# Kernel optimization log

Hardware: AMD Instinct MI355X
Metric: run time of the kernel (lower is better)

Reference implementation:

```python
import jax, jax.numpy as jnp
import numpy as np
import math

EMBED_DIM = 1024
NUM_HEADS = 16
HEAD_DIM = EMBED_DIM // NUM_HEADS
ROPE_BASE = 10000.0


def _rope_cache(seq_len, dim, dtype=jnp.float32):
    inv_freq = 1.0 / (ROPE_BASE ** (jnp.arange(0, dim, 2, dtype=jnp.float32) / dim))
    t = jnp.arange(seq_len, dtype=jnp.float32)
    freqs = t[:, None] * inv_freq[None, :]          # [S, D/2]
    emb = jnp.concatenate([freqs, freqs], axis=-1)  # [S, D]
    return jnp.cos(emb).astype(dtype), jnp.sin(emb).astype(dtype)


def _rotate_half(x):
    x1, x2 = jnp.split(x, 2, axis=-1)
    return jnp.concatenate([-x2, x1], axis=-1)


def setup_inputs() -> dict:
    key = jax.random.key(0)
    ks = jax.random.split(key, 12)
    B, S, E = 2, 2048, EMBED_DIM
    s = 1.0 / math.sqrt(E)
    inp = {
        "query": jax.random.normal(ks[0], (B, S, E), jnp.float32),
        "key": jax.random.normal(ks[1], (B, S, E), jnp.float32),
        "value": jax.random.normal(ks[2], (B, S, E), jnp.float32),
        "Wq": jax.random.normal(ks[3], (E, E), jnp.float32) * s,
        "bq": jnp.zeros((E,), jnp.float32),
        "Wk": jax.random.normal(ks[4], (E, E), jnp.float32) * s,
        "bk": jnp.zeros((E,), jnp.float32),
        "Wv": jax.random.normal(ks[5], (E, E), jnp.float32) * s,
        "bv": jnp.zeros((E,), jnp.float32),
        "Wo": jax.random.normal(ks[6], (E, E), jnp.float32) * s,
        "bo": jnp.zeros((E,), jnp.float32),
    }
    return inp


def reference(query, key, value, Wq, bq, Wk, bk, Wv, bv, Wo, bo):
    B, S, E = query.shape
    H, D = NUM_HEADS, HEAD_DIM

    def proj(x, W, b):  # torch Linear: x @ W.T + b -> [B,H,S,D]
        return (x @ W.T + b).reshape(B, -1, H, D).transpose(0, 2, 1, 3)

    q = proj(query, Wq, bq)
    k = proj(key, Wk, bk)
    v = proj(value, Wv, bv)

    cos, sin = _rope_cache(S, D, q.dtype)  # [S, D]
    cos = cos[None, None]                  # [1,1,S,D]
    sin = sin[None, None]
    q = q * cos + _rotate_half(q) * sin
    k = k * cos + _rotate_half(k) * sin

    scale = 1.0 / math.sqrt(D)
    scores = jnp.einsum("bhsd,bhtd->bhst", q, k) * scale  # [B,H,S,S]
    causal = jnp.triu(jnp.ones((S, S), bool), k=1)
    scores = jnp.where(causal[None, None], -jnp.inf, scores)
    attn = jax.nn.softmax(scores, axis=-1)
    out = jnp.einsum("bhst,bhtd->bhsd", attn, v)           # [B,H,S,D]
    out = out.transpose(0, 2, 1, 3).reshape(B, S, E)
    return out @ Wo.T + bo
```

## Files before the change

kernel.cpp:

```cpp
#include <hip/hip_runtime.h>
#include <math.h>

typedef unsigned short u16;
typedef __attribute__((ext_vector_type(4))) float f32x4;
typedef __attribute__((ext_vector_type(8))) short bf16x8;

#define SEQ   2048
#define EMB   1024
#define NH    16
#define HD    64
#define MROWS 4096

__device__ __forceinline__ u16 f2b(float f) {
    unsigned u = __float_as_uint(f);
    u += 0x7fff + ((u >> 16) & 1);
    return (u16)(u >> 16);
}
__device__ __forceinline__ unsigned pack_bf16x2(float a, float b) {
    unsigned ua = __float_as_uint(a) + 0x8000u;
    unsigned ub = __float_as_uint(b) + 0x8000u;
    return __builtin_amdgcn_perm(ub, ua, 0x07060302u);
}
__device__ __forceinline__ void gld16(const u16* g, const u16* l) {
    __builtin_amdgcn_global_load_lds((const __attribute__((address_space(1))) void*)g,
                                     (__attribute__((address_space(3))) void*)l, 16, 0, 0);
}

struct F2BArgs { const float* s[7]; u16* d[7]; };

__global__ void k_f2b(F2BArgs a) {
    int id = blockIdx.x;
    const float* src; u16* dst; int base;
    if (id < 6144) {
        int z = id >> 11;
        src = a.s[z]; dst = a.d[z];
        base = (id & 2047) << 8;
    } else {
        int r = id - 6144;
        int z = 3 + (r >> 9);
        src = a.s[z]; dst = a.d[z];
        base = (r & 511) << 8;
    }
    int i = base + threadIdx.x;
    const float4* s4 = (const float4*)src;
    float4 x = s4[i * 2], y = s4[i * 2 + 1];
    union { u16 u[8]; uint4 v; } o;
    o.u[0] = f2b(x.x); o.u[1] = f2b(x.y); o.u[2] = f2b(x.z); o.u[3] = f2b(x.w);
    o.u[4] = f2b(y.x); o.u[5] = f2b(y.y); o.u[6] = f2b(y.z); o.u[7] = f2b(y.w);
    ((uint4*)dst)[i] = o.v;
}

struct GemmArgs {
    const u16* A; const u16* Bw; const float* bias; u16* Cb;
};

__global__ __launch_bounds__(512, 2) void k_gemm_qkv(GemmArgs g0, GemmArgs g1, GemmArgs g2) {
    __shared__ u16 sbuf[3][24576];

    int id = blockIdx.x;
    int x = id / 48;
    int rem = id % 48;
    int z = rem >> 4;
    int y = rem & 15;
    GemmArgs g = (z == 0) ? g0 : (z == 1 ? g1 : g2);

    int tid = threadIdx.x;
    int wave = tid >> 6, lane = tid & 63, quad = lane >> 4, l16 = lane & 15;
    int wm = wave >> 1, wn = wave & 1;
    int m0 = y * 256, n0 = x * 128;
    const int K = EMB;

    auto stage = [&](int k0, u16* buf) {
#pragma unroll
        for (int pp = 0; pp < 6; pp++) {
            int slot = pp * 512 + tid;
            const u16* gsrc;
            if (pp < 4) {
                int row = slot >> 3, p = slot & 7;
                int c = p ^ (row & 7);
                gsrc = g.A + (size_t)(m0 + row) * K + k0 + c * 8;
            } else {
                int s2 = slot - 2048;
                int row = s2 >> 3, p = s2 & 7;
                int c = p ^ (row & 7);
                gsrc = g.Bw + (size_t)(n0 + row) * K + k0 + c * 8;
            }
            gld16(gsrc, buf + slot * 8);
        }
    };

    f32x4 acc[4][4];
#pragma unroll
    for (int i = 0; i < 4; i++)
#pragma unroll
        for (int j = 0; j < 4; j++) acc[i][j] = (f32x4){0.f, 0.f, 0.f, 0.f};

    int nt = K >> 6;
    stage(0, &sbuf[0][0]);
    stage(64, &sbuf[1][0]);
    for (int t = 0; t < nt; ++t) {
        if (t < nt - 1) asm volatile("s_waitcnt vmcnt(6)" ::: "memory");
        else            asm volatile("s_waitcnt vmcnt(0)" ::: "memory");
        asm volatile("s_barrier" ::: "memory");
        if (t + 2 < nt) stage((t + 2) << 6, &sbuf[0][0] + ((t + 2) % 3) * 24576);

        const u16* Ab = &sbuf[0][0] + (t % 3) * 24576;
        const u16* Bb = Ab + 16384;
#pragma unroll
        for (int kk = 0; kk < 2; kk++) {
            bf16x8 af[4], bfr[4];
#pragma unroll
            for (int i = 0; i < 4; i++) {
                int row = wm * 64 + i * 16 + l16;
                af[i] = *(const bf16x8*)&Ab[row * 64 + (((kk << 2) | quad) ^ (row & 7)) * 8];
            }
#pragma unroll
            for (int j = 0; j < 4; j++) {
                int row = wn * 64 + j * 16 + l16;
                bfr[j] = *(const bf16x8*)&Bb[row * 64 + (((kk << 2) | quad) ^ (row & 7)) * 8];
            }
#pragma unroll
            for (int i = 0; i < 4; i++)
#pragma unroll
                for (int j = 0; j < 4; j++)
                    acc[i][j] = __builtin_amdgcn_mfma_f32_16x16x32_bf16(af[i], bfr[j], acc[i][j], 0, 0, 0);
        }
    }

    if (z < 2) {
        float qscale = (z == 0) ? 0.18033688011112042f : 1.0f;
#pragma unroll
        for (int j = 0; j < 2; j++) {
            int col1 = n0 + wn * 64 + j * 16 + l16;
            int dd1 = col1 & 63;
            int h = col1 >> 6;
            float inv = __expf(-(float)dd1 * 0.28782313662425575f);
            float b1 = g.bias[col1], b2 = g.bias[col1 + 32];
#pragma unroll
            for (int i = 0; i < 4; i++)
#pragma unroll
                for (int r = 0; r < 4; r++) {
                    int row = m0 + wm * 64 + i * 16 + quad * 4 + r;
                    int b = row >> 11, s = row & (SEQ - 1);
                    float sn, cs;
                    __sincosf((float)s * inv, &sn, &cs);
                    float x1 = acc[i][j][r] + b1;
                    float x2 = acc[i][j + 2][r] + b2;
                    size_t base = ((size_t)(b * NH + h) * SEQ + s) << 6;
                    g.Cb[base + dd1]      = f2b((x1 * cs - x2 * sn) * qscale);
                    g.Cb[base + dd1 + 32] = f2b((x2 * cs + x1 * sn) * qscale);
                }
        }
    } else {
        __syncthreads();
        u16* tr = &sbuf[0][0] + wave * 4096;
        int h = (n0 >> 6) + wn;
        int b = m0 >> 11;
        int s0 = (m0 & (SEQ - 1)) + wm * 64;
#pragma unroll
        for (int j = 0; j < 4; j++) {
            float bv = g.bias[n0 + wn * 64 + j * 16 + l16];
#pragma unroll
            for (int i = 0; i < 4; i++) {
                uint2 pk;
                pk.x = pack_bf16x2(acc[i][j][0] + bv, acc[i][j][1] + bv);
                pk.y = pack_bf16x2(acc[i][j][2] + bv, acc[i][j][3] + bv);
                int row = j * 16 + l16;
                int c4 = i * 4 + quad;
                *(uint2*)&tr[row * 64 + ((c4 ^ (row & 14)) << 2)] = pk;
            }
        }
        u16* dst = g.Cb + (((size_t)(b * NH + h) * HD) * SEQ) + s0;
#pragma unroll
        for (int ps = 0; ps < 8; ps++) {
            int d = ps * 8 + (lane >> 3);
            int c4 = (lane & 7) * 2;
            uint4 v = *(const uint4*)&tr[d * 64 + ((c4 ^ (d & 14)) << 2)];
            *(uint4*)&dst[(size_t)d * SEQ + c4 * 4] = v;
        }
    }
}

__global__ __launch_bounds__(256) void k_gemm_o(const u16* __restrict__ A,
                                                const u16* __restrict__ Bw,
                                                const float* __restrict__ bias,
                                                float* __restrict__ C) {
    __shared__ u16 sb[2][6144];
    int tid = threadIdx.x;
    int w = tid >> 6, lane = tid & 63, quad = lane >> 4, l16 = lane & 15;
    int y = blockIdx.x & 63, x = blockIdx.x >> 6;
    int m0 = y * 64, n0 = x * 128;
    const int K = EMB;

    auto stage = [&](int k0, u16* buf) {
#pragma unroll
        for (int pp = 0; pp < 3; pp++) {
            int slot = pp * 256 + tid;
            if (slot < 256) {
                int row = slot >> 2, p = slot & 3;
                int c = p ^ (row & 3);
                gld16(A + (size_t)(m0 + row) * K + k0 + c * 8, buf + slot * 8);
            } else {
                int s2 = slot - 256;
                int row = s2 >> 2, p = s2 & 3;
                int c = p ^ (row & 3);
                gld16(Bw + (size_t)(n0 + row) * K + k0 + c * 8, buf + 2048 + s2 * 8);
            }
        }
    };

    f32x4 acc[4][2];
#pragma unroll
    for (int i = 0; i < 4; i++)
#pragma unroll
        for (int j = 0; j < 2; j++) acc[i][j] = (f32x4){0.f, 0.f, 0.f, 0.f};

    int nk = K >> 5;
    stage(0, sb[0]);
    for (int ks = 0; ks < nk; ks++) {
        __syncthreads();
        if (ks + 1 < nk) stage((ks + 1) << 5, sb[(ks + 1) & 1]);
        const u16* Ab = sb[ks & 1];
        const u16* Bb = Ab + 2048;
        bf16x8 af[4], bf[2];
#pragma unroll
        for (int i = 0; i < 4; i++) {
            int row = i * 16 + l16;
            af[i] = *(const bf16x8*)&Ab[row * 32 + (quad ^ (row & 3)) * 8];
        }
#pragma unroll
        for (int j = 0; j < 2; j++) {
            int row = w * 32 + j * 16 + l16;
            bf[j] = *(const bf16x8*)&Bb[row * 32 + (quad ^ (row & 3)) * 8];
        }
#pragma unroll
        for (int i = 0; i < 4; i++)
#pragma unroll
            for (int j = 0; j < 2; j++)
                acc[i][j] = __builtin_amdgcn_mfma_f32_16x16x32_bf16(af[i], bf[j], acc[i][j], 0, 0, 0);
    }

#pragma unroll
    for (int i = 0; i < 4; i++)
#pragma unroll
        for (int r = 0; r < 4; r++) {
            int row = m0 + i * 16 + quad * 4 + r;
#pragma unroll
            for (int j = 0; j < 2; j++) {
                int col = n0 + w * 32 + j * 16 + l16;
                C[(size_t)row * EMB + col] = acc[i][j][r] + bias[col];
            }
        }
}

__global__ __launch_bounds__(512, 2) void k_attn(const u16* __restrict__ Q,
                                                 const u16* __restrict__ K,
                                                 const u16* __restrict__ Vt,
                                                 u16* __restrict__ O) {
    __shared__ u16 kv[4][8192];
    __shared__ u16 Pl[8][1024];
    int tid = threadIdx.x;
    int w = tid >> 6, lane = tid & 63, quad = lane >> 4, l16 = lane & 15;
    int pair = w & 3, par = w >> 2;
    int bh = blockIdx.x & 31;
    int qt = 15 - (blockIdx.x >> 5);
    int q0w = qt * 128 + pair * 32;

    const u16* Qb = Q + (size_t)bh * SEQ * HD;
    const u16* Kb = K + (size_t)bh * SEQ * HD;
    const u16* Vb = Vt + (size_t)bh * HD * SEQ;
    u16* pl = Pl[w];

    auto stage = [&](int t0, u16* buf) {
#pragma unroll
        for (int pp = 0; pp < 2; pp++) {
            int slot = pp * 512 + tid;
            int r = (slot >> 3) & 63;
            int p = slot & 7;
            int c = p ^ (r & 7);
            const u16* gsrc = (pp < 1) ? Kb + (size_t)(t0 + r) * HD + c * 8
                                       : Vb + (size_t)r * SEQ + t0 + c * 8;
            gld16(gsrc, buf + slot * 8);
        }
    };

    bf16x8 bq[2][2];
#pragma unroll
    for (int g = 0; g < 2; g++) {
        size_t base = (size_t)(q0w + g * 16 + l16) * HD + quad * 8;
        bq[g][0] = *(const bf16x8*)&Qb[base];
        bq[g][1] = *(const bf16x8*)&Qb[base + 32];
    }

    f32x4 o2[2][4];
#pragma unroll
    for (int g = 0; g < 2; g++)
#pragma unroll
        for (int jd = 0; jd < 4; jd++) o2[g][jd] = (f32x4){0.f, 0.f, 0.f, 0.f};
    float l_p[2] = {0.f, 0.f};

    int nsup = qt + 1;
    stage(0, kv[0]);
    stage(64, kv[2]);
    for (int k = 0; k < nsup; ++k) {
        __syncthreads();
        if (k + 1 < nsup) {
            stage((k + 1) * 128,      kv[(k + 1) & 1]);
            stage((k + 1) * 128 + 64, kv[2 + ((k + 1) & 1)]);
        }
        int t0 = k * 128 + par * 64;
        if (t0 > q0w + 31) continue;

        const u16* Kl = kv[par * 2 + (k & 1)];
        const u16* Vl = Kl + 4096;

        bf16x8 kf[4][2], vf[4][2];
#pragma unroll
        for (int mt = 0; mt < 4; mt++) {
            int row = mt * 16 + l16;
            kf[mt][0] = *(const bf16x8*)&Kl[row * 64 + (quad ^ (row & 7)) * 8];
            kf[mt][1] = *(const bf16x8*)&Kl[row * 64 + ((quad + 4) ^ (row & 7)) * 8];
            vf[mt][0] = *(const bf16x8*)&Vl[row * 64 + (quad ^ (row & 7)) * 8];
            vf[mt][1] = *(const bf16x8*)&Vl[row * 64 + ((quad + 4) ^ (row & 7)) * 8];
        }

#pragma unroll
        for (int g = 0; g < 2; g++) {
            int qmin = q0w + g * 16;
            if (t0 > qmin + 15) continue;

            f32x4 sc[4];
#pragma unroll
            for (int mt = 0; mt < 4; mt++) {
                sc[mt] = (f32x4){0.f, 0.f, 0.f, 0.f};
                sc[mt] = __builtin_amdgcn_mfma_f32_16x16x32_bf16(kf[mt][0], bq[g][0], sc[mt], 0, 0, 0);
                sc[mt] = __builtin_amdgcn_mfma_f32_16x16x32_bf16(kf[mt][1], bq[g][1], sc[mt], 0, 0, 0);
            }

            if (t0 + 63 > qmin) {
                int q = qmin + l16;
#pragma unroll
                for (int mt = 0; mt < 4; mt++)
#pragma unroll
                    for (int r = 0; r < 4; r++) {
                        int t = t0 + mt * 16 + quad * 4 + r;
                        if (t > q) sc[mt][r] = -INFINITY;
                    }
            }

            float rs = 0.f;
#pragma unroll
            for (int mt = 0; mt < 4; mt++)
#pragma unroll
                for (int r = 0; r < 4; r++) {
                    float p = __builtin_amdgcn_exp2f(sc[mt][r] - 64.f);
                    sc[mt][r] = p;
                    rs += p;
                }
            l_p[g] += rs;

#pragma unroll
            for (int mt = 0; mt < 4; mt++) {
                uint2 pk;
                pk.x = pack_bf16x2(sc[mt][0], sc[mt][1]);
                pk.y = pack_bf16x2(sc[mt][2], sc[mt][3]);
                int chunk = 2 * mt + (quad >> 1);
                *(uint2*)&pl[l16 * 64 + (chunk ^ (l16 & 7)) * 8 + (quad & 1) * 4] = pk;
            }

            bf16x8 pb0 = *(const bf16x8*)&pl[l16 * 64 + (quad ^ (l16 & 7)) * 8];
            bf16x8 pb1 = *(const bf16x8*)&pl[l16 * 64 + ((quad + 4) ^ (l16 & 7)) * 8];

#pragma unroll
            for (int jd = 0; jd < 4; jd++) {
                o2[g][jd] = __builtin_amdgcn_mfma_f32_16x16x32_bf16(vf[jd][0], pb0, o2[g][jd], 0, 0, 0);
                o2[g][jd] = __builtin_amdgcn_mfma_f32_16x16x32_bf16(vf[jd][1], pb1, o2[g][jd], 0, 0, 0);
            }
        }
    }

    __syncthreads();
    float* mp = (float*)&kv[0][0] + pair * 2176;
    if (par) {
#pragma unroll
        for (int g = 0; g < 2; g++) {
#pragma unroll
            for (int jd = 0; jd < 4; jd++)
                *(f32x4*)&mp[(g * 4 + jd) * 256 + lane * 4] = o2[g][jd];
            mp[2048 + g * 64 + lane] = l_p[g];
        }
    }
    __syncthreads();
    if (par) return;
#pragma unroll
    for (int g = 0; g < 2; g++) {
#pragma unroll
        for (int jd = 0; jd < 4; jd++)
            o2[g][jd] += *(const f32x4*)&mp[(g * 4 + jd) * 256 + lane * 4];
        l_p[g] += mp[2048 + g * 64 + lane];
    }

    u16* ep = ((u16*)&kv[0][0]) + 18432 + pair * 1216;
    int b = bh >> 4, h = bh & (NH - 1);
#pragma unroll
    for (int g = 0; g < 2; g++) {
        float l = l_p[g];
        l += __shfl_xor(l, 16, 64);
        l += __shfl_xor(l, 32, 64);
        float inv = 1.f / l;
#pragma unroll
        for (int jd = 0; jd < 4; jd++) {
            uint2 pk;
            pk.x = pack_bf16x2(o2[g][jd][0] * inv, o2[g][jd][1] * inv);
            pk.y = pack_bf16x2(o2[g][jd][2] * inv, o2[g][jd][3] * inv);
            *(uint2*)&ep[l16 * 72 + jd * 16 + quad * 4] = pk;
        }
        int row = lane >> 2, dc = (lane & 3) * 16;
        uint4 d0 = *(const uint4*)&ep[row * 72 + dc];
        uint4 d1 = *(const uint4*)&ep[row * 72 + dc + 8];
        int q = q0w + g * 16 + row;
        size_t addr = (size_t)(b * SEQ + q) * EMB + h * HD + dc;
        *(uint4*)&O[addr] = d0;
        *(uint4*)&O[addr + 8] = d1;
    }
}

extern "C" void kernel_launch(void* const* d_in, const int* in_sizes, int n_in,
                              void* d_out, int out_size, void* d_ws, size_t ws_size,
                              hipStream_t stream) {
    const float* query = (const float*)d_in[0];
    const float* key_  = (const float*)d_in[1];
    const float* value = (const float*)d_in[2];
    const float* Wq = (const float*)d_in[3];
    const float* bq = (const float*)d_in[4];
    const float* Wk = (const float*)d_in[5];
    const float* bk = (const float*)d_in[6];
    const float* Wv = (const float*)d_in[7];
    const float* bv = (const float*)d_in[8];
    const float* Wo = (const float*)d_in[9];
    const float* bo = (const float*)d_in[10];
    float* out = (float*)d_out;

    char* ws = (char*)d_ws;
    const size_t MB = 1u << 20;
    u16* xq  = (u16*)(ws + 0 * MB);
    u16* xk  = (u16*)(ws + 8 * MB);
    u16* xv  = (u16*)(ws + 16 * MB);
    u16* wqb = (u16*)(ws + 24 * MB);
    u16* wkb = (u16*)(ws + 26 * MB);
    u16* wvb = (u16*)(ws + 28 * MB);
    u16* wob = (u16*)(ws + 30 * MB);
    u16* Qp  = (u16*)(ws + 32 * MB);
    u16* Kp  = (u16*)(ws + 40 * MB);
    u16* Vt  = (u16*)(ws + 48 * MB);
    u16* Ab  = xk;

    F2BArgs fa;
    fa.s[0] = query; fa.s[1] = key_; fa.s[2] = value;
    fa.s[3] = Wq; fa.s[4] = Wk; fa.s[5] = Wv; fa.s[6] = Wo;
    fa.d[0] = xq; fa.d[1] = xk; fa.d[2] = xv;
    fa.d[3] = wqb; fa.d[4] = wkb; fa.d[5] = wvb; fa.d[6] = wob;
    k_f2b<<<8192, 256, 0, stream>>>(fa);

    GemmArgs gq = { xq, wqb, bq, Qp };
    GemmArgs gk = { xk, wkb, bk, Kp };
    GemmArgs gv = { xv, wvb, bv, Vt };
    k_gemm_qkv<<<384, 512, 0, stream>>>(gq, gk, gv);

    k_attn<<<512, 512, 0, stream>>>(Qp, Kp, Vt, Ab);

    k_gemm_o<<<512, 256, 0, stream>>>(Ab, wob, bo, out);
}
```

Before: 205.3 us.

## Enlarge QKV GEMM tile to 256x256 with double buffering and precomputed RoPE table

The QKV projection GEMM tile grows from 256x128 to 256x256, so each of the 8 waves now computes 128x64, and the grid halves to 192 blocks. The LDS pipeline changes from triple to double buffering with an extra barrier per k-step, and s_setprio is raised around the MFMA block. RoPE cos/sin values are now precomputed into a table by extra blocks in the conversion kernel, replacing the per-element sincos in the epilogue. The larger tile improves operand reuse but leaves fewer blocks than CUs (192 blocks on a 256-CU part) and raises register pressure.

```diff
diff --git a/kernel.cpp b/kernel.cpp
--- a/kernel.cpp
+++ b/kernel.cpp
@@ -26,10 +26,22 @@
                                      (__attribute__((address_space(3))) void*)l, 16, 0, 0);
 }
 
-struct F2BArgs { const float* s[7]; u16* d[7]; };
+struct F2BArgs { const float* s[7]; u16* d[7]; float2* tbl; };
 
 __global__ void k_f2b(F2BArgs a) {
     int id = blockIdx.x;
+    if (id >= 8192) {
+        int base = ((id - 8192) * 256 + threadIdx.x) * 4;
+#pragma unroll
+        for (int e = 0; e < 4; e++) {
+            int idx = base + e;
+            int s = idx >> 5, d = idx & 31;
+            float inv = __expf(-(float)d * 0.28782313662425575f);
+            float ang = (float)s * inv;
+            a.tbl[idx] = make_float2(cosf(ang), sinf(ang));
+        }
+        return;
+    }
     const float* src; u16* dst; int base;
     if (id < 6144) {
         int z = id >> 11;
@@ -51,11 +63,11 @@
 }
 
 struct GemmArgs {
-    const u16* A; const u16* Bw; const float* bias; u16* Cb;
+    const u16* A; const u16* Bw; const float* bias; u16* Cb; const float2* rope;
 };
 
 __global__ __launch_bounds__(512, 2) void k_gemm_qkv(GemmArgs g0, GemmArgs g1, GemmArgs g2) {
-    __shared__ u16 sbuf[3][24576];
+    __shared__ u16 sbuf[2][32768];
 
     int id = blockIdx.x;
     int x = id / 48;
@@ -66,13 +78,13 @@
 
     int tid = threadIdx.x;
     int wave = tid >> 6, lane = tid & 63, quad = lane >> 4, l16 = lane & 15;
-    int wm = wave >> 1, wn = wave & 1;
-    int m0 = y * 256, n0 = x * 128;
+    int wm = wave >> 2, wn = wave & 3;
+    int m0 = y * 256, n0 = x * 256;
     const int K = EMB;
 
     auto stage = [&](int k0, u16* buf) {
 #pragma unroll
-        for (int pp = 0; pp < 6; pp++) {
+        for (int pp = 0; pp < 8; pp++) {
             int slot = pp * 512 + tid;
             const u16* gsrc;
             if (pp < 4) {
@@ -89,29 +101,31 @@
         }
     };
 
-    f32x4 acc[4][4];
-#pragma unroll
-    for (int i = 0; i < 4; i++)
+    f32x4 acc[8][4];
+#pragma unroll
+    for (int i = 0; i < 8; i++)
 #pragma unroll
         for (int j = 0; j < 4; j++) acc[i][j] = (f32x4){0.f, 0.f, 0.f, 0.f};
 
     int nt = K >> 6;
     stage(0, &sbuf[0][0]);
-    stage(64, &sbuf[1][0]);
     for (int t = 0; t < nt; ++t) {
-        if (t < nt - 1) asm volatile("s_waitcnt vmcnt(6)" ::: "memory");
-        else            asm volatile("s_waitcnt vmcnt(0)" ::: "memory");
+        if (t + 1 < nt) {
+            stage((t + 1) << 6, &sbuf[(t + 1) & 1][0]);
+            asm volatile("s_waitcnt vmcnt(8)" ::: "memory");
+        } else {
+            asm volatile("s_waitcnt vmcnt(0)" ::: "memory");
+        }
         asm volatile("s_barrier" ::: "memory");
-        if (t + 2 < nt) stage((t + 2) << 6, &sbuf[0][0] + ((t + 2) % 3) * 24576);
-
-        const u16* Ab = &sbuf[0][0] + (t % 3) * 24576;
+
+        const u16* Ab = &sbuf[t & 1][0];
         const u16* Bb = Ab + 16384;
 #pragma unroll
         for (int kk = 0; kk < 2; kk++) {
-            bf16x8 af[4], bfr[4];
-#pragma unroll
-            for (int i = 0; i < 4; i++) {
-                int row = wm * 64 + i * 16 + l16;
+            bf16x8 af[8], bfr[4];
+#pragma unroll
+            for (int i = 0; i < 8; i++) {
+                int row = wm * 128 + i * 16 + l16;
                 af[i] = *(const bf16x8*)&Ab[row * 64 + (((kk << 2) | quad) ^ (row & 7)) * 8];
             }
 #pragma unroll
@@ -119,12 +133,15 @@
                 int row = wn * 64 + j * 16 + l16;
                 bfr[j] = *(const bf16x8*)&Bb[row * 64 + (((kk << 2) | quad) ^ (row & 7)) * 8];
             }
-#pragma unroll
-            for (int i = 0; i < 4; i++)
+            __builtin_amdgcn_s_setprio(1);
+#pragma unroll
+            for (int i = 0; i < 8; i++)
 #pragma unroll
                 for (int j = 0; j < 4; j++)
                     acc[i][j] = __builtin_amdgcn_mfma_f32_16x16x32_bf16(af[i], bfr[j], acc[i][j], 0, 0, 0);
-        }
+            __builtin_amdgcn_s_setprio(0);
+        }
+        asm volatile("s_barrier" ::: "memory");
     }
 
     if (z < 2) {
@@ -134,48 +151,46 @@
             int col1 = n0 + wn * 64 + j * 16 + l16;
             int dd1 = col1 & 63;
             int h = col1 >> 6;
-            float inv = __expf(-(float)dd1 * 0.28782313662425575f);
             float b1 = g.bias[col1], b2 = g.bias[col1 + 32];
 #pragma unroll
-            for (int i = 0; i < 4; i++)
+            for (int i = 0; i < 8; i++)
 #pragma unroll
                 for (int r = 0; r < 4; r++) {
-                    int row = m0 + wm * 64 + i * 16 + quad * 4 + r;
+                    int row = m0 + wm * 128 + i * 16 + quad * 4 + r;
                     int b = row >> 11, s = row & (SEQ - 1);
-                    float sn, cs;
-                    __sincosf((float)s * inv, &sn, &cs);
+                    float2 cs = g.rope[s * 32 + dd1];
                     float x1 = acc[i][j][r] + b1;
                     float x2 = acc[i][j + 2][r] + b2;
                     size_t base = ((size_t)(b * NH + h) * SEQ + s) << 6;
-                    g.Cb[base + dd1]      = f2b((x1 * cs - x2 * sn) * qscale);
-                    g.Cb[base + dd1 + 32] = f2b((x2 * cs + x1 * sn) * qscale);
+                    g.Cb[base + dd1]      = f2b((x1 * cs.x - x2 * cs.y) * qscale);
+                    g.Cb[base + dd1 + 32] = f2b((x2 * cs.x + x1 * cs.y) * qscale);
                 }
         }
     } else {
         __syncthreads();
-        u16* tr = &sbuf[0][0] + wave * 4096;
+        u16* tr = &sbuf[0][0] + wave * 8192;
         int h = (n0 >> 6) + wn;
         int b = m0 >> 11;
-        int s0 = (m0 & (SEQ - 1)) + wm * 64;
+        int s0 = (m0 & (SEQ - 1)) + wm * 128;
 #pragma unroll
         for (int j = 0; j < 4; j++) {
             float bv = g.bias[n0 + wn * 64 + j * 16 + l16];
 #pragma unroll
-            for (int i = 0; i < 4; i++) {
+            for (int i = 0; i < 8; i++) {
                 uint2 pk;
                 pk.x = pack_bf16x2(acc[i][j][0] + bv, acc[i][j][1] + bv);
                 pk.y = pack_bf16x2(acc[i][j][2] + bv, acc[i][j][3] + bv);
                 int row = j * 16 + l16;
                 int c4 = i * 4 + quad;
-                *(uint2*)&tr[row * 64 + ((c4 ^ (row & 14)) << 2)] = pk;
+                *(uint2*)&tr[row * 128 + ((c4 ^ (row & 30)) << 2)] = pk;
             }
         }
         u16* dst = g.Cb + (((size_t)(b * NH + h) * HD) * SEQ) + s0;
 #pragma unroll
-        for (int ps = 0; ps < 8; ps++) {
-            int d = ps * 8 + (lane >> 3);
-            int c4 = (lane & 7) * 2;
-            uint4 v = *(const uint4*)&tr[d * 64 + ((c4 ^ (d & 14)) << 2)];
+        for (int ps = 0; ps < 16; ps++) {
+            int d = ps * 4 + (lane >> 4);
+            int c4 = (lane & 15) * 2;
+            uint4 v = *(const uint4*)&tr[d * 128 + ((c4 ^ (d & 30)) << 2)];
             *(uint4*)&dst[(size_t)d * SEQ + c4 * 4] = v;
         }
     }
@@ -453,6 +468,7 @@
     u16* Qp  = (u16*)(ws + 32 * MB);
     u16* Kp  = (u16*)(ws + 40 * MB);
     u16* Vt  = (u16*)(ws + 48 * MB);
+    float2* tbl = (float2*)(ws + 56 * MB);
     u16* Ab  = xk;
 
     F2BArgs fa;
@@ -460,12 +476,13 @@
     fa.s[3] = Wq; fa.s[4] = Wk; fa.s[5] = Wv; fa.s[6] = Wo;
     fa.d[0] = xq; fa.d[1] = xk; fa.d[2] = xv;
     fa.d[3] = wqb; fa.d[4] = wkb; fa.d[5] = wvb; fa.d[6] = wob;
-    k_f2b<<<8192, 256, 0, stream>>>(fa);
-
-    GemmArgs gq = { xq, wqb, bq, Qp };
-    GemmArgs gk = { xk, wkb, bk, Kp };
-    GemmArgs gv = { xv, wvb, bv, Vt };
-    k_gemm_qkv<<<384, 512, 0, stream>>>(gq, gk, gv);
+    fa.tbl = tbl;
+    k_f2b<<<8256, 256, 0, stream>>>(fa);
+
+    GemmArgs gq = { xq, wqb, bq, Qp, tbl };
+    GemmArgs gk = { xk, wkb, bk, Kp, tbl };
+    GemmArgs gv = { xv, wvb, bv, Vt, tbl };
+    k_gemm_qkv<<<192, 512, 0, stream>>>(gq, gk, gv);
 
     k_attn<<<512, 512, 0, stream>>>(Qp, Kp, Vt, Ab);
 
```

Result: slower. 216.1 us (+5.2%).

## Fuse fp32-to-bf16 activation conversion into QKV GEMM A-tile loading

Applied to the files above, without the earlier changes.

The separate conversion pass for query/key/value is removed. The QKV GEMM now reads fp32 activations straight into registers, rounds them to bf16 and writes them to LDS, while weights still stream in through direct global-to-LDS loads. The pipeline drops from three LDS stages to two with register prefetch, uses __syncthreads per tile, lowers the launch-bounds occupancy hint to 1, and raises wave priority around the MFMA block. This avoids writing and re-reading 24 MB of bf16 activations, at the cost of more register pressure and a shallower pipeline inside the GEMM.

```diff
diff --git a/kernel.cpp b/kernel.cpp
--- a/kernel.cpp
+++ b/kernel.cpp
@@ -16,6 +16,9 @@
     u += 0x7fff + ((u >> 16) & 1);
     return (u16)(u >> 16);
 }
+__device__ __forceinline__ unsigned pack_rne(float a, float b) {
+    return (unsigned)f2b(a) | ((unsigned)f2b(b) << 16);
+}
 __device__ __forceinline__ unsigned pack_bf16x2(float a, float b) {
     unsigned ua = __float_as_uint(a) + 0x8000u;
     unsigned ub = __float_as_uint(b) + 0x8000u;
@@ -26,22 +29,14 @@
                                      (__attribute__((address_space(3))) void*)l, 16, 0, 0);
 }
 
-struct F2BArgs { const float* s[7]; u16* d[7]; };
+struct F2BArgs { const float* s[4]; u16* d[4]; };
 
 __global__ void k_f2b(F2BArgs a) {
     int id = blockIdx.x;
-    const float* src; u16* dst; int base;
-    if (id < 6144) {
-        int z = id >> 11;
-        src = a.s[z]; dst = a.d[z];
-        base = (id & 2047) << 8;
-    } else {
-        int r = id - 6144;
-        int z = 3 + (r >> 9);
-        src = a.s[z]; dst = a.d[z];
-        base = (r & 511) << 8;
-    }
-    int i = base + threadIdx.x;
+    int z = id >> 9;
+    const float* src = a.s[z];
+    u16* dst = a.d[z];
+    int i = ((id & 511) << 8) + threadIdx.x;
     const float4* s4 = (const float4*)src;
     float4 x = s4[i * 2], y = s4[i * 2 + 1];
     union { u16 u[8]; uint4 v; } o;
@@ -51,11 +46,11 @@
 }
 
 struct GemmArgs {
-    const u16* A; const u16* Bw; const float* bias; u16* Cb;
+    const float* A; const u16* Bw; const float* bias; u16* Cb;
 };
 
-__global__ __launch_bounds__(512, 2) void k_gemm_qkv(GemmArgs g0, GemmArgs g1, GemmArgs g2) {
-    __shared__ u16 sbuf[3][24576];
+__global__ __launch_bounds__(512, 1) void k_gemm_qkv(GemmArgs g0, GemmArgs g1, GemmArgs g2) {
+    __shared__ u16 sbuf[2][24576];
 
     int id = blockIdx.x;
     int x = id / 48;
@@ -70,24 +65,40 @@
     int m0 = y * 256, n0 = x * 128;
     const int K = EMB;
 
-    auto stage = [&](int k0, u16* buf) {
-#pragma unroll
-        for (int pp = 0; pp < 6; pp++) {
+    float4 ar[4][2];
+    auto issueA = [&](int k0) {
+#pragma unroll
+        for (int pp = 0; pp < 4; pp++) {
             int slot = pp * 512 + tid;
-            const u16* gsrc;
-            if (pp < 4) {
-                int row = slot >> 3, p = slot & 7;
-                int c = p ^ (row & 7);
-                gsrc = g.A + (size_t)(m0 + row) * K + k0 + c * 8;
-            } else {
-                int s2 = slot - 2048;
-                int row = s2 >> 3, p = s2 & 7;
-                int c = p ^ (row & 7);
-                gsrc = g.Bw + (size_t)(n0 + row) * K + k0 + c * 8;
-            }
-            gld16(gsrc, buf + slot * 8);
+            int row = slot >> 3, p = slot & 7;
+            int c = p ^ (row & 7);
+            const float* src = g.A + (size_t)(m0 + row) * K + k0 + c * 8;
+            ar[pp][0] = *(const float4*)src;
+            ar[pp][1] = *(const float4*)(src + 4);
         }
     };
+    auto writeA = [&](u16* buf) {
+#pragma unroll
+        for (int pp = 0; pp < 4; pp++) {
+            int slot = pp * 512 + tid;
+            uint4 o;
+            o.x = pack_rne(ar[pp][0].x, ar[pp][0].y);
+            o.y = pack_rne(ar[pp][0].z, ar[pp][0].w);
+            o.z = pack_rne(ar[pp][1].x, ar[pp][1].y);
+            o.w = pack_rne(ar[pp][1].z, ar[pp][1].w);
+            *(uint4*)(buf + slot * 8) = o;
+        }
+    };
+    auto issueB = [&](int k0, u16* buf) {
+#pragma unroll
+        for (int pp = 4; pp < 6; pp++) {
+            int slot = pp * 512 + tid;
+            int s2 = slot - 2048;
+            int row = s2 >> 3, p = s2 & 7;
+            int c = p ^ (row & 7);
+            gld16(g.Bw + (size_t)(n0 + row) * K + k0 + c * 8, buf + slot * 8);
+        }
+    };
 
     f32x4 acc[4][4];
 #pragma unroll
@@ -96,16 +107,20 @@
         for (int j = 0; j < 4; j++) acc[i][j] = (f32x4){0.f, 0.f, 0.f, 0.f};
 
     int nt = K >> 6;
-    stage(0, &sbuf[0][0]);
-    stage(64, &sbuf[1][0]);
+    issueA(0);
+    issueB(0, &sbuf[0][0]);
+    writeA(&sbuf[0][0]);
+    __syncthreads();
+
     for (int t = 0; t < nt; ++t) {
-        if (t < nt - 1) asm volatile("s_waitcnt vmcnt(6)" ::: "memory");
-        else            asm volatile("s_waitcnt vmcnt(0)" ::: "memory");
-        asm volatile("s_barrier" ::: "memory");
-        if (t + 2 < nt) stage((t + 2) << 6, &sbuf[0][0] + ((t + 2) % 3) * 24576);
-
-        const u16* Ab = &sbuf[0][0] + (t % 3) * 24576;
-        const u16* Bb = Ab + 16384;
+        u16* cur = &sbuf[t & 1][0];
+        u16* nxt = &sbuf[(t + 1) & 1][0];
+        if (t + 1 < nt) {
+            issueA((t + 1) << 6);
+            issueB((t + 1) << 6, nxt);
+        }
+        const u16* Ab = cur;
+        const u16* Bb = cur + 16384;
 #pragma unroll
         for (int kk = 0; kk < 2; kk++) {
             bf16x8 af[4], bfr[4];
@@ -119,12 +134,16 @@
                 int row = wn * 64 + j * 16 + l16;
                 bfr[j] = *(const bf16x8*)&Bb[row * 64 + (((kk << 2) | quad) ^ (row & 7)) * 8];
             }
+            __builtin_amdgcn_s_setprio(1);
 #pragma unroll
             for (int i = 0; i < 4; i++)
 #pragma unroll
                 for (int j = 0; j < 4; j++)
                     acc[i][j] = __builtin_amdgcn_mfma_f32_16x16x32_bf16(af[i], bfr[j], acc[i][j], 0, 0, 0);
-        }
+            __builtin_amdgcn_s_setprio(0);
+        }
+        if (t + 1 < nt) writeA(nxt);
+        __syncthreads();
     }
 
     if (z < 2) {
@@ -443,9 +462,7 @@
 
     char* ws = (char*)d_ws;
     const size_t MB = 1u << 20;
-    u16* xq  = (u16*)(ws + 0 * MB);
-    u16* xk  = (u16*)(ws + 8 * MB);
-    u16* xv  = (u16*)(ws + 16 * MB);
+    u16* Ab  = (u16*)(ws + 8 * MB);
     u16* wqb = (u16*)(ws + 24 * MB);
     u16* wkb = (u16*)(ws + 26 * MB);
     u16* wvb = (u16*)(ws + 28 * MB);
@@ -453,18 +470,15 @@
     u16* Qp  = (u16*)(ws + 32 * MB);
     u16* Kp  = (u16*)(ws + 40 * MB);
     u16* Vt  = (u16*)(ws + 48 * MB);
-    u16* Ab  = xk;
 
     F2BArgs fa;
-    fa.s[0] = query; fa.s[1] = key_; fa.s[2] = value;
-    fa.s[3] = Wq; fa.s[4] = Wk; fa.s[5] = Wv; fa.s[6] = Wo;
-    fa.d[0] = xq; fa.d[1] = xk; fa.d[2] = xv;
-    fa.d[3] = wqb; fa.d[4] = wkb; fa.d[5] = wvb; fa.d[6] = wob;
-    k_f2b<<<8192, 256, 0, stream>>>(fa);
-
-    GemmArgs gq = { xq, wqb, bq, Qp };
-    GemmArgs gk = { xk, wkb, bk, Kp };
-    GemmArgs gv = { xv, wvb, bv, Vt };
+    fa.s[0] = Wq; fa.s[1] = Wk; fa.s[2] = Wv; fa.s[3] = Wo;
+    fa.d[0] = wqb; fa.d[1] = wkb; fa.d[2] = wvb; fa.d[3] = wob;
+    k_f2b<<<2048, 256, 0, stream>>>(fa);
+
+    GemmArgs gq = { query, wqb, bq, Qp };
+    GemmArgs gk = { key_,  wkb, bk, Kp };
+    GemmArgs gv = { value, wvb, bv, Vt };
     k_gemm_qkv<<<384, 512, 0, stream>>>(gq, gk, gv);
 
     k_attn<<<512, 512, 0, stream>>>(Qp, Kp, Vt, Ab);
```

Result: slower. 229.9 us (+12.0%).
